# Kernel tuning notes

Measured on AMD Instinct MI355X. Metric: run time of the kernel, lower is better.

The kernel has to match this reference:

```python
import jax, jax.numpy as jnp
import numpy as np

HEADS = 16
DIM_HEAD = 64
SCALE = DIM_HEAD ** -0.5


def setup_inputs() -> dict:
    key = jax.random.key(0)
    k1, k2, k3, k4 = jax.random.split(key, 4)
    b, n, dim = 2, 2048, 1024
    inner = HEADS * DIM_HEAD
    x = jax.random.normal(k1, (b, n, dim), dtype=jnp.float32)
    mask = jax.random.randint(k2, (b, n), 0, 2, dtype=jnp.int32)
    w_qkv = jax.random.normal(k3, (3 * inner, dim), dtype=jnp.float32) * (dim ** -0.5)
    w_out = jax.random.normal(k4, (dim, inner), dtype=jnp.float32) * (inner ** -0.5)
    return {"x": x, "mask": mask, "w_qkv": w_qkv, "w_out": w_out}


def reference(x, mask, w_qkv, w_out):
    b, n, dim = x.shape
    # qkv projection (no bias), split into q,k,v and reshape b n (h d) -> b h n d
    qkv = jnp.einsum('bnd,ed->bne', x, w_qkv)
    q, k, v = jnp.split(qkv, 3, axis=-1)
    def to_heads(t):
        return t.reshape(b, n, HEADS, DIM_HEAD).transpose(0, 2, 1, 3)
    q, k, v = to_heads(q), to_heads(k), to_heads(v)
    # scores [b,h,n,n]
    dots = jnp.einsum('bhid,bhjd->bhij', q, k) * SCALE
    # pairwise mask: mask_i * mask_j, broadcast over heads
    pair = (mask[:, :, None] * mask[:, None, :])[:, None, :, :]  # [b,1,n,n]
    neg = -jnp.finfo(dots.dtype).max
    dots = jnp.where(pair == 0, neg, dots)
    attn = jax.nn.softmax(dots, axis=-1)
    out = jnp.einsum('bhij,bhjd->bhid', attn, v)
    out = out.transpose(0, 2, 1, 3).reshape(b, n, HEADS * DIM_HEAD)
    return jnp.einsum('bne,de->bnd', out, w_out)
```

## Files before the change

### kernel.cpp

```cpp
#include <hip/hip_runtime.h>
#include <stdint.h>

typedef unsigned short u16;
typedef uint32_t u32;
typedef __attribute__((ext_vector_type(8))) short bf8;
typedef __attribute__((ext_vector_type(4))) float f4;
typedef __attribute__((ext_vector_type(16))) float f16f;
typedef __attribute__((ext_vector_type(4))) unsigned short us4;

__device__ __forceinline__ u16 f2bf(float f) {
    uint32_t u = __float_as_uint(f);
    u += 0x7FFF + ((u >> 16) & 1);
    return (u16)(u >> 16);
}
__device__ __forceinline__ float bf2f(u16 v) {
    return __uint_as_float(((uint32_t)v) << 16);
}
__device__ __forceinline__ void gld_lds16(const u16* g, u16* l) {
    __builtin_amdgcn_global_load_lds(
        (const __attribute__((address_space(1))) void*)g,
        (__attribute__((address_space(3))) void*)l, 16, 0, 0);
}
__device__ __forceinline__ f16f mfma32(bf8 a, bf8 b, f16f c) {
    return __builtin_amdgcn_mfma_f32_32x32x16_bf16(a, b, c, 0, 0, 0);
}
__device__ __forceinline__ u32 cvtpk(float lo, float hi) {
    u32 r; asm("v_cvt_pk_bf16_f32 %0, %1, %2" : "=v"(r) : "v"(lo), "v"(hi)); return r;
}
__device__ __forceinline__ void plswap(u32& a, u32& b) {
    asm("v_permlane32_swap_b32 %0, %1" : "+v"(a), "+v"(b));
}
__device__ __forceinline__ float fexp2(float x) {
    float r; asm("v_exp_f32 %0, %1" : "=v"(r) : "v"(x)); return r;
}

struct alignas(8) US4 { u16 a, b, c, d; };

__global__ void cvt_all(const float* __restrict__ x, const float* __restrict__ wqkv,
                        const float* __restrict__ wout,
                        u16* __restrict__ xbf, u16* __restrict__ wqkvbf, u16* __restrict__ woutbf) {
    int i = blockIdx.x * blockDim.x + threadIdx.x;
    const float* src; u16* dst; int off;
    if (i < 1048576)      { src = x;    dst = xbf;    off = i; }
    else if (i < 1835008) { src = wqkv; dst = wqkvbf; off = i - 1048576; }
    else                  { src = wout; dst = woutbf; off = i - 1835008; }
    float4 v = ((const float4*)src)[off];
    US4 o; o.a = f2bf(v.x); o.b = f2bf(v.y); o.c = f2bf(v.z); o.d = f2bf(v.w);
    ((US4*)dst)[off] = o;
}

__global__ __launch_bounds__(256)
void gemm_qkv(const u16* __restrict__ A, const u16* __restrict__ W,
              u16* __restrict__ Qo, u16* __restrict__ Ko, u16* __restrict__ Vo)
{
    __shared__ __align__(16) u16 lsmem[2 * 128 * 64];
    u16* lA = lsmem;
    u16* lB = lsmem + 128 * 64;
    const int tid = threadIdx.x;
    const int lane = tid & 63, wid = tid >> 6;
    const int g = lane >> 4, c = lane & 15;
    const int bid = blockIdx.x;
    const int wg = (bid & 7) * 96 + (bid >> 3);
    const int m0 = (wg / 24) * 128, n0 = (wg % 24) * 128;
    const int wr = wid >> 1, wc = wid & 1;

    f4 acc[4][4];
#pragma unroll
    for (int i = 0; i < 4; ++i)
#pragma unroll
        for (int j = 0; j < 4; ++j) { acc[i][j][0] = 0.f; acc[i][j][1] = 0.f; acc[i][j][2] = 0.f; acc[i][j][3] = 0.f; }

    for (int k0 = 0; k0 < 1024; k0 += 64) {
        __syncthreads();
#pragma unroll
        for (int i = 0; i < 4; ++i) {
            int chunk = i * 256 + tid;
            int row = chunk >> 3, cc = chunk & 7;
            int gc = cc ^ (row & 7);
            gld_lds16(A + (m0 + row) * 1024 + k0 + gc * 8, lA + (i * 256 + wid * 64) * 8);
            gld_lds16(W + (n0 + row) * 1024 + k0 + gc * 8, lB + (i * 256 + wid * 64) * 8);
        }
        __syncthreads();
#pragma unroll
        for (int kk = 0; kk < 2; ++kk) {
            bf8 af[4], bfr[4];
#pragma unroll
            for (int mi = 0; mi < 4; ++mi) {
                int row = wr * 64 + mi * 16 + c;
                af[mi] = *(const bf8*)&lA[row * 64 + ((kk * 4 + g) ^ (row & 7)) * 8];
            }
#pragma unroll
            for (int ni = 0; ni < 4; ++ni) {
                int row = wc * 64 + ni * 16 + c;
                bfr[ni] = *(const bf8*)&lB[row * 64 + ((kk * 4 + g) ^ (row & 7)) * 8];
            }
#pragma unroll
            for (int mi = 0; mi < 4; ++mi)
#pragma unroll
                for (int ni = 0; ni < 4; ++ni)
                    acc[mi][ni] = __builtin_amdgcn_mfma_f32_16x16x32_bf16(af[mi], bfr[ni], acc[mi][ni], 0, 0, 0);
        }
    }

    __syncthreads();
    u16* eb = lsmem + wid * 4096;
    const int e0 = n0 + wc * 64;
    const int part = e0 >> 10;
    const int hh = (e0 & 1023) >> 6;
    const float scale = (part == 0) ? 0.18033688011112042f : 1.0f;

    if (part < 2) {
#pragma unroll
        for (int mi = 0; mi < 4; ++mi)
#pragma unroll
            for (int ni = 0; ni < 4; ++ni) {
                int colL = ni * 16 + c;
#pragma unroll
                for (int r = 0; r < 4; ++r) {
                    int tokL = mi * 16 + g * 4 + r;
                    int chk = ((colL >> 3) ^ (tokL & 7));
                    eb[tokL * 64 + chk * 8 + (colL & 7)] = f2bf(acc[mi][ni][r] * scale);
                }
            }
        u16* dst0 = (part == 0) ? Qo : Ko;
#pragma unroll
        for (int i = 0; i < 8; ++i) {
            int row = i * 8 + (lane >> 3);
            int ch = lane & 7;
            bf8 v = *(const bf8*)&eb[row * 64 + ((ch ^ (row & 7)) << 3)];
            int tok = m0 + wr * 64 + row;
            int bb = tok >> 11, nn = tok & 2047;
            *(bf8*)&dst0[((bb * 16 + hh) * 2048 + nn) * 64 + ch * 8] = v;
        }
    } else {
#pragma unroll
        for (int mi = 0; mi < 4; ++mi)
#pragma unroll
            for (int ni = 0; ni < 4; ++ni) {
                int dL = ni * 16 + c;
                int tokL0 = mi * 16 + g * 4;
                int tchk = ((tokL0 >> 3) ^ (dL & 7));
                us4 w;
                w[0] = f2bf(acc[mi][ni][0]); w[1] = f2bf(acc[mi][ni][1]);
                w[2] = f2bf(acc[mi][ni][2]); w[3] = f2bf(acc[mi][ni][3]);
                *(us4*)&eb[dL * 64 + tchk * 8 + (tokL0 & 7)] = w;
            }
#pragma unroll
        for (int i = 0; i < 8; ++i) {
            int dr = i * 8 + (lane >> 3);
            int ch = lane & 7;
            bf8 v = *(const bf8*)&eb[dr * 64 + ((ch ^ (dr & 7)) << 3)];
            int tok0 = m0 + wr * 64 + ch * 8;
            int bb = tok0 >> 11, nn = tok0 & 2047;
            *(bf8*)&Vo[((bb * 16 + hh) * 64 + dr) * 2048 + nn] = v;
        }
    }
}

__global__ void vmean_kernel(const u16* __restrict__ VT, float* __restrict__ vpart) {
    const int blk = blockIdx.x;
    const int bh = blk >> 3, seg = blk & 7;
    const int tid = threadIdx.x;
    const int d = tid >> 2, sub = tid & 3;
    const u16* row = VT + bh * 131072 + d * 2048 + seg * 256 + sub * 64;
    float s = 0.f;
#pragma unroll
    for (int i = 0; i < 64; i += 8) {
        bf8 v = *(const bf8*)&row[i];
#pragma unroll
        for (int j = 0; j < 8; ++j) s += bf2f((u16)v[j]);
    }
    __shared__ float red[256];
    red[tid] = s;
    __syncthreads();
    if (sub == 0)
        vpart[blk * 64 + d] = red[tid] + red[tid + 1] + red[tid + 2] + red[tid + 3];
}

__global__ __launch_bounds__(512, 4)
void attn_kernel(const u16* __restrict__ Q, const u16* __restrict__ K, const u16* __restrict__ VT,
                 const int* __restrict__ mask, const float* __restrict__ vpart,
                 u16* __restrict__ O)
{
    __shared__ __align__(16) u16 lS[2][2][8192];
    __shared__ u16 lBias[2048];

    const int tid = threadIdx.x;
    const int lane = tid & 63, wid = tid >> 6;
    const int q = lane & 31, hi = lane >> 5;
    const int half = wid >> 2, qw = wid & 3;
    const int B = blockIdx.x;
    const int xcd = B & 7, idx = B >> 3;
    const int bh = xcd * 4 + (idx & 3), qt = idx >> 2;
    const int b = bh >> 4, h = bh & 15;
    const u16* Qb = Q + bh * (2048 * 64);
    const u16* Kb = K + bh * (2048 * 64);
    const u16* Vb = VT + bh * (64 * 2048);

    const u16 NEGB = f2bf(-1e30f);
    for (int i = tid; i < 2048; i += 512)
        lBias[i] = mask[b * 2048 + i] ? (u16)0 : NEGB;

    const int qrow = qt * 128 + qw * 32 + q;
    bf8 qf[4];
#pragma unroll
    for (int s = 0; s < 4; ++s)
        qf[s] = *(const bf8*)&Qb[qrow * 64 + s * 16 + hi * 8];

    f16f oacc[2];
#pragma unroll
    for (int i = 0; i < 16; ++i) { oacc[0][i] = 0.f; oacc[1][i] = 0.f; }
    const float mrun = 20.0f;
    float lrun = 0.f;

    bf8 oneb;
#pragma unroll
    for (int i = 0; i < 8; ++i) oneb[i] = 0;
    if (hi == 0) oneb[0] = (short)0x3F80;

    const int sl = tid & 255;
    const int r0 = sl >> 3,         c0 = (sl & 7) ^ (r0 & 7);
    const int r1 = (sl + 256) >> 3, c1 = ((sl + 256) & 7) ^ (r1 & 7);
    const int tile0 = half * 16;

    {
        u16* bp = &lS[half][0][0];
        gld_lds16(Kb + (tile0 * 64 + r0) * 64 + c0 * 8, bp + sl * 8);
        gld_lds16(Kb + (tile0 * 64 + r1) * 64 + c1 * 8, bp + (sl + 256) * 8);
        gld_lds16(Vb + r0 * 2048 + tile0 * 64 + c0 * 8, bp + 4096 + sl * 8);
        gld_lds16(Vb + r1 * 2048 + tile0 * 64 + c1 * 8, bp + 4096 + (sl + 256) * 8);
    }
    __syncthreads();

    for (int t = 0; t < 16; ++t) {
        const int cur = t & 1;
        if (t < 15) {
            const int tn = tile0 + t + 1;
            u16* bn = &lS[half][cur ^ 1][0];
            gld_lds16(Kb + (tn * 64 + r0) * 64 + c0 * 8, bn + sl * 8);
            gld_lds16(Kb + (tn * 64 + r1) * 64 + c1 * 8, bn + (sl + 256) * 8);
            gld_lds16(Vb + r0 * 2048 + tn * 64 + c0 * 8, bn + 4096 + sl * 8);
            gld_lds16(Vb + r1 * 2048 + tn * 64 + c1 * 8, bn + 4096 + (sl + 256) * 8);
        }
        const u16* kbuf = &lS[half][cur][0];
        const u16* vbuf = kbuf + 4096;
        const int tt = tile0 + t;

        f16f st[2];
#pragma unroll
        for (int kb = 0; kb < 2; ++kb) {
            bf8 ba;
#pragma unroll
            for (int i = 0; i < 8; ++i) ba[i] = 0;
            if (hi == 0) ba[0] = (short)lBias[tt * 64 + kb * 32 + q];
            f16f z;
#pragma unroll
            for (int i = 0; i < 16; ++i) z[i] = 0.f;
            st[kb] = mfma32(ba, oneb, z);
            const int row = kb * 32 + q;
#pragma unroll
            for (int s = 0; s < 4; ++s) {
                bf8 kf = *(const bf8*)&kbuf[row * 64 + (((2 * s + hi) ^ (row & 7)) << 3)];
                st[kb] = mfma32(kf, qf[s], st[kb]);
            }
        }

#pragma unroll
        for (int kb = 0; kb < 2; ++kb)
#pragma unroll
            for (int i = 0; i < 16; ++i)
                st[kb][i] = fexp2(st[kb][i] - mrun);
        float sx[16];
#pragma unroll
        for (int i = 0; i < 16; ++i) sx[i] = st[0][i] + st[1][i];
#pragma unroll
        for (int i = 0; i < 8; ++i) sx[i] += sx[i + 8];
#pragma unroll
        for (int i = 0; i < 4; ++i) sx[i] += sx[i + 4];
        lrun += (sx[0] + sx[1]) + (sx[2] + sx[3]);

        bf8 pa[4];
#pragma unroll
        for (int kb = 0; kb < 2; ++kb)
#pragma unroll
            for (int gp = 0; gp < 2; ++gp) {
                u32 a0 = cvtpk(st[kb][gp * 8 + 0], st[kb][gp * 8 + 1]);
                u32 a1 = cvtpk(st[kb][gp * 8 + 2], st[kb][gp * 8 + 3]);
                u32 b0 = cvtpk(st[kb][gp * 8 + 4], st[kb][gp * 8 + 5]);
                u32 b1 = cvtpk(st[kb][gp * 8 + 6], st[kb][gp * 8 + 7]);
                plswap(a0, b0);
                plswap(a1, b1);
                union { bf8 v; u32 u[4]; } pu;
                pu.u[0] = a0; pu.u[1] = a1; pu.u[2] = b0; pu.u[3] = b1;
                pa[kb * 2 + gp] = pu.v;
            }

#pragma unroll
        for (int db = 0; db < 2; ++db) {
            const int vrow = db * 32 + q;
#pragma unroll
            for (int s = 0; s < 4; ++s) {
                bf8 vf = *(const bf8*)&vbuf[vrow * 64 + (((2 * s + hi) ^ (vrow & 7)) << 3)];
                oacc[db] = mfma32(vf, pa[s], oacc[db]);
            }
        }
        __syncthreads();
    }

    lrun += __shfl_xor(lrun, 32);

    float* mb = (float*)&lS[0][0][0];
    float* mp = mb + (qw * 64 + lane) * 35;
    if (half == 1) {
        mp[0] = mrun; mp[1] = lrun;
#pragma unroll
        for (int i = 0; i < 16; ++i) { mp[2 + i] = oacc[0][i]; mp[18 + i] = oacc[1][i]; }
    }
    __syncthreads();
    if (half == 0) {
        float m2 = mp[0], l2 = mp[1];
        float mm = fmaxf(mrun, m2);
        float e1 = fexp2(mrun - mm), e2 = fexp2(m2 - mm);
        float inv = 1.0f / (lrun * e1 + l2 * e2);
        float a1 = e1 * inv, a2 = e2 * inv;
        u16* eb = ((u16*)&lS[0][0][0]) + 20480 + qw * 2432;
#pragma unroll
        for (int db = 0; db < 2; ++db)
#pragma unroll
            for (int q2 = 0; q2 < 4; ++q2) {
                us4 w;
#pragma unroll
                for (int j = 0; j < 4; ++j) {
                    int i = q2 * 4 + j;
                    w[j] = f2bf(oacc[db][i] * a1 + mp[2 + db * 16 + i] * a2);
                }
                *(us4*)&eb[q * 76 + db * 32 + q2 * 8 + hi * 4] = w;
            }
#pragma unroll
        for (int i = 0; i < 4; ++i) {
            int row = i * 8 + (lane >> 3);
            int ch = lane & 7;
            bf8 v = *(const bf8*)&eb[row * 76 + ch * 8];
            int tok = qt * 128 + qw * 32 + row;
            if (lBias[tok] != 0) {
                f4 s0 = { 0.f, 0.f, 0.f, 0.f }, s1 = { 0.f, 0.f, 0.f, 0.f };
#pragma unroll
                for (int sg = 0; sg < 8; ++sg) {
                    const f4* vp = (const f4*)(vpart + (bh * 8 + sg) * 64 + ch * 8);
                    s0 += vp[0]; s1 += vp[1];
                }
                const float sc = 1.0f / 2048.0f;
                v[0] = (short)f2bf(s0[0] * sc); v[1] = (short)f2bf(s0[1] * sc);
                v[2] = (short)f2bf(s0[2] * sc); v[3] = (short)f2bf(s0[3] * sc);
                v[4] = (short)f2bf(s1[0] * sc); v[5] = (short)f2bf(s1[1] * sc);
                v[6] = (short)f2bf(s1[2] * sc); v[7] = (short)f2bf(s1[3] * sc);
            }
            *(bf8*)&O[(b * 2048 + tok) * 1024 + h * 64 + ch * 8] = v;
        }
    }
}

__global__ __launch_bounds__(256)
void gemm_out(const u16* __restrict__ A, const u16* __restrict__ W, float* __restrict__ out)
{
    __shared__ __align__(16) u16 lA[128 * 64];
    __shared__ __align__(16) u16 lB[64 * 64];
    const int tid = threadIdx.x;
    const int lane = tid & 63, wid = tid >> 6;
    const int g = lane >> 4, c = lane & 15;
    const int bid = blockIdx.x;
    const int wg = (bid & 7) * 64 + (bid >> 3);
    const int m0 = (wg >> 4) * 128, n0 = (wg & 15) * 64;
    const int wr = wid >> 1, wc = wid & 1;

    f4 acc[4][2];
#pragma unroll
    for (int i = 0; i < 4; ++i)
#pragma unroll
        for (int j = 0; j < 2; ++j) { acc[i][j][0] = 0.f; acc[i][j][1] = 0.f; acc[i][j][2] = 0.f; acc[i][j][3] = 0.f; }

    for (int k0 = 0; k0 < 1024; k0 += 64) {
        __syncthreads();
#pragma unroll
        for (int i = 0; i < 4; ++i) {
            int chunk = i * 256 + tid;
            int row = chunk >> 3, cc = chunk & 7;
            int gc = cc ^ (row & 7);
            gld_lds16(A + (m0 + row) * 1024 + k0 + gc * 8, lA + (i * 256 + wid * 64) * 8);
        }
#pragma unroll
        for (int i = 0; i < 2; ++i) {
            int chunk = i * 256 + tid;
            int row = chunk >> 3, cc = chunk & 7;
            int gc = cc ^ (row & 7);
            gld_lds16(W + (n0 + row) * 1024 + k0 + gc * 8, lB + (i * 256 + wid * 64) * 8);
        }
        __syncthreads();
#pragma unroll
        for (int kk = 0; kk < 2; ++kk) {
            bf8 af[4], bfr[2];
#pragma unroll
            for (int mi = 0; mi < 4; ++mi) {
                int row = wr * 64 + mi * 16 + c;
                af[mi] = *(const bf8*)&lA[row * 64 + ((kk * 4 + g) ^ (row & 7)) * 8];
            }
#pragma unroll
            for (int ni = 0; ni < 2; ++ni) {
                int row = wc * 32 + ni * 16 + c;
                bfr[ni] = *(const bf8*)&lB[row * 64 + ((kk * 4 + g) ^ (row & 7)) * 8];
            }
#pragma unroll
            for (int mi = 0; mi < 4; ++mi)
#pragma unroll
                for (int ni = 0; ni < 2; ++ni)
                    acc[mi][ni] = __builtin_amdgcn_mfma_f32_16x16x32_bf16(af[mi], bfr[ni], acc[mi][ni], 0, 0, 0);
        }
    }
#pragma unroll
    for (int mi = 0; mi < 4; ++mi) {
        int row0 = m0 + wr * 64 + mi * 16 + g * 4;
#pragma unroll
        for (int ni = 0; ni < 2; ++ni) {
            int col = n0 + wc * 32 + ni * 16 + c;
#pragma unroll
            for (int r = 0; r < 4; ++r)
                out[(row0 + r) * 1024 + col] = acc[mi][ni][r];
        }
    }
}

extern "C" void kernel_launch(void* const* d_in, const int* in_sizes, int n_in,
                              void* d_out, int out_size, void* d_ws, size_t ws_size,
                              hipStream_t stream) {
    const float* x    = (const float*)d_in[0];
    const int*   mask = (const int*)d_in[1];
    const float* wqkv = (const float*)d_in[2];
    const float* wout = (const float*)d_in[3];
    float* out = (float*)d_out;

    u16* ws = (u16*)d_ws;
    u16* xbf    = ws;
    u16* wqkvbf = xbf + 4096 * 1024;
    u16* woutbf = wqkvbf + 3072 * 1024;
    u16* qb     = woutbf + 1024 * 1024;
    u16* kb     = qb + 2 * 16 * 2048 * 64;
    u16* vtb    = kb + 2 * 16 * 2048 * 64;
    float* vpart = (float*)(vtb + 2 * 16 * 2048 * 64);
    u16* ob = xbf;

    cvt_all<<<8192, 256, 0, stream>>>(x, wqkv, wout, xbf, wqkvbf, woutbf);
    gemm_qkv<<<768, 256, 0, stream>>>(xbf, wqkvbf, qb, kb, vtb);
    vmean_kernel<<<256, 256, 0, stream>>>(vtb, vpart);
    attn_kernel<<<512, 512, 0, stream>>>(qb, kb, vtb, mask, vpart, ob);
    gemm_out<<<512, 256, 0, stream>>>(ob, woutbf, out);
}
```

Baseline: 123.3 us.

## Halve KV tile to 32 keys to cut LDS and raise attention occupancy

Shrinks the per-iteration key/value tile from 64 to 32 keys, which halves the LDS staging buffers and the score registers, and doubles the loop trip count. Launch bounds rise from 4 to 8 waves-per-EU hint so more blocks can be resident at once. The epilogue merge is simplified because both halves share the fixed max, so the exp rescale is dropped, at the cost of one extra barrier. The risk is more barriers and loop overhead per key, and smaller MFMA batches per sync.

```diff
diff --git a/kernel.cpp b/kernel.cpp
--- a/kernel.cpp
+++ b/kernel.cpp
@@ -177,13 +177,13 @@
         vpart[blk * 64 + d] = red[tid] + red[tid + 1] + red[tid + 2] + red[tid + 3];
 }
 
-__global__ __launch_bounds__(512, 4)
+__global__ __launch_bounds__(512, 8)
 void attn_kernel(const u16* __restrict__ Q, const u16* __restrict__ K, const u16* __restrict__ VT,
                  const int* __restrict__ mask, const float* __restrict__ vpart,
                  u16* __restrict__ O)
 {
-    __shared__ __align__(16) u16 lS[2][2][8192];
-    __shared__ u16 lBias[2048];
+    __shared__ __align__(16) u16 lAll[16896 + 2048];
+    u16* lBias = &lAll[16896];
 
     const int tid = threadIdx.x;
     const int lane = tid & 63, wid = tid >> 6;
@@ -219,88 +219,76 @@
     if (hi == 0) oneb[0] = (short)0x3F80;
 
     const int sl = tid & 255;
-    const int r0 = sl >> 3,         c0 = (sl & 7) ^ (r0 & 7);
-    const int r1 = (sl + 256) >> 3, c1 = ((sl + 256) & 7) ^ (r1 & 7);
-    const int tile0 = half * 16;
+    const int krow = sl >> 3, kgc = (sl & 7) ^ (krow & 7);
+    const int vrow = sl >> 2, vgc = (sl & 3) ^ (vrow & 3);
+    const int tile0 = half * 32;
 
     {
-        u16* bp = &lS[half][0][0];
-        gld_lds16(Kb + (tile0 * 64 + r0) * 64 + c0 * 8, bp + sl * 8);
-        gld_lds16(Kb + (tile0 * 64 + r1) * 64 + c1 * 8, bp + (sl + 256) * 8);
-        gld_lds16(Vb + r0 * 2048 + tile0 * 64 + c0 * 8, bp + 4096 + sl * 8);
-        gld_lds16(Vb + r1 * 2048 + tile0 * 64 + c1 * 8, bp + 4096 + (sl + 256) * 8);
+        u16* bp = &lAll[(half * 2 + 0) * 4096];
+        gld_lds16(Kb + (tile0 * 32 + krow) * 64 + kgc * 8, bp + sl * 8);
+        gld_lds16(Vb + vrow * 2048 + tile0 * 32 + vgc * 8, bp + 2048 + sl * 8);
     }
     __syncthreads();
 
-    for (int t = 0; t < 16; ++t) {
+    for (int t = 0; t < 32; ++t) {
         const int cur = t & 1;
-        if (t < 15) {
+        if (t < 31) {
             const int tn = tile0 + t + 1;
-            u16* bn = &lS[half][cur ^ 1][0];
-            gld_lds16(Kb + (tn * 64 + r0) * 64 + c0 * 8, bn + sl * 8);
-            gld_lds16(Kb + (tn * 64 + r1) * 64 + c1 * 8, bn + (sl + 256) * 8);
-            gld_lds16(Vb + r0 * 2048 + tn * 64 + c0 * 8, bn + 4096 + sl * 8);
-            gld_lds16(Vb + r1 * 2048 + tn * 64 + c1 * 8, bn + 4096 + (sl + 256) * 8);
-        }
-        const u16* kbuf = &lS[half][cur][0];
-        const u16* vbuf = kbuf + 4096;
+            u16* bn = &lAll[(half * 2 + (cur ^ 1)) * 4096];
+            gld_lds16(Kb + (tn * 32 + krow) * 64 + kgc * 8, bn + sl * 8);
+            gld_lds16(Vb + vrow * 2048 + tn * 32 + vgc * 8, bn + 2048 + sl * 8);
+        }
+        const u16* kbuf = &lAll[(half * 2 + cur) * 4096];
+        const u16* vbuf = kbuf + 2048;
         const int tt = tile0 + t;
 
-        f16f st[2];
-#pragma unroll
-        for (int kb = 0; kb < 2; ++kb) {
+        f16f st;
+        {
             bf8 ba;
 #pragma unroll
             for (int i = 0; i < 8; ++i) ba[i] = 0;
-            if (hi == 0) ba[0] = (short)lBias[tt * 64 + kb * 32 + q];
+            if (hi == 0) ba[0] = (short)lBias[tt * 32 + q];
             f16f z;
 #pragma unroll
             for (int i = 0; i < 16; ++i) z[i] = 0.f;
-            st[kb] = mfma32(ba, oneb, z);
-            const int row = kb * 32 + q;
+            st = mfma32(ba, oneb, z);
 #pragma unroll
             for (int s = 0; s < 4; ++s) {
-                bf8 kf = *(const bf8*)&kbuf[row * 64 + (((2 * s + hi) ^ (row & 7)) << 3)];
-                st[kb] = mfma32(kf, qf[s], st[kb]);
-            }
-        }
-
-#pragma unroll
-        for (int kb = 0; kb < 2; ++kb)
-#pragma unroll
-            for (int i = 0; i < 16; ++i)
-                st[kb][i] = fexp2(st[kb][i] - mrun);
-        float sx[16];
-#pragma unroll
-        for (int i = 0; i < 16; ++i) sx[i] = st[0][i] + st[1][i];
-#pragma unroll
-        for (int i = 0; i < 8; ++i) sx[i] += sx[i + 8];
+                bf8 kf = *(const bf8*)&kbuf[q * 64 + (((2 * s + hi) ^ (q & 7)) << 3)];
+                st = mfma32(kf, qf[s], st);
+            }
+        }
+
+#pragma unroll
+        for (int i = 0; i < 16; ++i)
+            st[i] = fexp2(st[i] - mrun);
+        float sx[8];
+#pragma unroll
+        for (int i = 0; i < 8; ++i) sx[i] = st[i] + st[i + 8];
 #pragma unroll
         for (int i = 0; i < 4; ++i) sx[i] += sx[i + 4];
         lrun += (sx[0] + sx[1]) + (sx[2] + sx[3]);
 
-        bf8 pa[4];
-#pragma unroll
-        for (int kb = 0; kb < 2; ++kb)
-#pragma unroll
-            for (int gp = 0; gp < 2; ++gp) {
-                u32 a0 = cvtpk(st[kb][gp * 8 + 0], st[kb][gp * 8 + 1]);
-                u32 a1 = cvtpk(st[kb][gp * 8 + 2], st[kb][gp * 8 + 3]);
-                u32 b0 = cvtpk(st[kb][gp * 8 + 4], st[kb][gp * 8 + 5]);
-                u32 b1 = cvtpk(st[kb][gp * 8 + 6], st[kb][gp * 8 + 7]);
-                plswap(a0, b0);
-                plswap(a1, b1);
-                union { bf8 v; u32 u[4]; } pu;
-                pu.u[0] = a0; pu.u[1] = a1; pu.u[2] = b0; pu.u[3] = b1;
-                pa[kb * 2 + gp] = pu.v;
-            }
+        bf8 pa[2];
+#pragma unroll
+        for (int gp = 0; gp < 2; ++gp) {
+            u32 a0 = cvtpk(st[gp * 8 + 0], st[gp * 8 + 1]);
+            u32 a1 = cvtpk(st[gp * 8 + 2], st[gp * 8 + 3]);
+            u32 b0 = cvtpk(st[gp * 8 + 4], st[gp * 8 + 5]);
+            u32 b1 = cvtpk(st[gp * 8 + 6], st[gp * 8 + 7]);
+            plswap(a0, b0);
+            plswap(a1, b1);
+            union { bf8 v; u32 u[4]; } pu;
+            pu.u[0] = a0; pu.u[1] = a1; pu.u[2] = b0; pu.u[3] = b1;
+            pa[gp] = pu.v;
+        }
 
 #pragma unroll
         for (int db = 0; db < 2; ++db) {
-            const int vrow = db * 32 + q;
-#pragma unroll
-            for (int s = 0; s < 4; ++s) {
-                bf8 vf = *(const bf8*)&vbuf[vrow * 64 + (((2 * s + hi) ^ (vrow & 7)) << 3)];
+            const int row = db * 32 + q;
+#pragma unroll
+            for (int s = 0; s < 2; ++s) {
+                bf8 vf = *(const bf8*)&vbuf[row * 32 + (((2 * s + hi) ^ (row & 3)) << 3)];
                 oacc[db] = mfma32(vf, pa[s], oacc[db]);
             }
         }
@@ -309,31 +297,33 @@
 
     lrun += __shfl_xor(lrun, 32);
 
-    float* mb = (float*)&lS[0][0][0];
-    float* mp = mb + (qw * 64 + lane) * 35;
+    float* mb = (float*)&lAll[0];
+    float* mp = mb + (qw * 64 + lane) * 33;
     if (half == 1) {
-        mp[0] = mrun; mp[1] = lrun;
-#pragma unroll
-        for (int i = 0; i < 16; ++i) { mp[2 + i] = oacc[0][i]; mp[18 + i] = oacc[1][i]; }
+        mp[0] = lrun;
+#pragma unroll
+        for (int i = 0; i < 16; ++i) { mp[1 + i] = oacc[0][i]; mp[17 + i] = oacc[1][i]; }
     }
     __syncthreads();
     if (half == 0) {
-        float m2 = mp[0], l2 = mp[1];
-        float mm = fmaxf(mrun, m2);
-        float e1 = fexp2(mrun - mm), e2 = fexp2(m2 - mm);
-        float inv = 1.0f / (lrun * e1 + l2 * e2);
-        float a1 = e1 * inv, a2 = e2 * inv;
-        u16* eb = ((u16*)&lS[0][0][0]) + 20480 + qw * 2432;
+        float inv = 1.0f / (lrun + mp[0]);
+#pragma unroll
+        for (int i = 0; i < 16; ++i) {
+            oacc[0][i] = (oacc[0][i] + mp[1 + i]) * inv;
+            oacc[1][i] = (oacc[1][i] + mp[17 + i]) * inv;
+        }
+    }
+    __syncthreads();
+    if (half == 0) {
+        u16* eb = &lAll[0] + qw * 2432;
 #pragma unroll
         for (int db = 0; db < 2; ++db)
 #pragma unroll
             for (int q2 = 0; q2 < 4; ++q2) {
                 us4 w;
 #pragma unroll
-                for (int j = 0; j < 4; ++j) {
-                    int i = q2 * 4 + j;
-                    w[j] = f2bf(oacc[db][i] * a1 + mp[2 + db * 16 + i] * a2);
-                }
+                for (int j = 0; j < 4; ++j)
+                    w[j] = f2bf(oacc[db][q2 * 4 + j]);
                 *(us4*)&eb[q * 76 + db * 32 + q2 * 8 + hi * 4] = w;
             }
 #pragma unroll
```

Result: slower. 233.3 us (+89.2%).
